# Performance work log

Measured on AMD Instinct MI355X. Metric: run time of the kernel, lower is better.

Reference implementation:

```python
import jax, jax.numpy as jnp
import numpy as np

B = 1024       # batch of triples
E = 50000      # num_entities
R = 500        # num_relations
D = 512        # dimension
P = 16         # parts
C = 8          # num_cores
ALPHA = 2.0    # -> q = alpha/2 = 1.0
Q = ALPHA / 2.0
DP = D // P    # 32


def setup_inputs() -> dict:
    key = jax.random.key(0)
    ks = jax.random.split(key, 10)
    xav_e = (2.0 / (E + D)) ** 0.5
    xav_r = (2.0 / (R + D)) ** 0.5
    return {
        "heads": jax.random.randint(ks[0], (B,), 0, E),
        "relations": jax.random.randint(ks[1], (B,), 0, R),
        "tails": jax.random.randint(ks[2], (B,), 0, E),
        "entity_w": jax.random.normal(ks[3], (E, D), dtype=jnp.float32) * xav_e,
        "relation_w": jax.random.normal(ks[4], (R, D), dtype=jnp.float32) * xav_r,
        "W_cores": jax.random.uniform(ks[5], (C, P, P, P), dtype=jnp.float32,
                                      minval=-0.01, maxval=0.01),
        "attn_w1": jax.random.normal(ks[6], (2 * D, D), dtype=jnp.float32) * (1.0 / (2 * D)) ** 0.5,
        "attn_b1": jnp.zeros((D,), dtype=jnp.float32),
        "attn_w2": jax.random.normal(ks[7], (D, C), dtype=jnp.float32) * (1.0 / D) ** 0.5,
        "attn_b2": jnp.zeros((C,), dtype=jnp.float32),
    }


def _pq_norm(x):
    # ((|x|^p).sum(2) ** q).sum(1), p=2
    return ((x * x).sum(2) ** Q).sum(1)


def _geometric_consistency(W_cores):
    # center of mass of |W| along each axis, per core; vectorized over cores
    coords = jnp.arange(P, dtype=jnp.float32)
    Wa = jnp.abs(W_cores)                      # [C,P,P,P]
    tot = Wa.sum(axis=(1, 2, 3))               # [C]
    cx = (Wa * coords[None, :, None, None]).sum(axis=(1, 2, 3)) / tot
    cy = (Wa * coords[None, None, :, None]).sum(axis=(1, 2, 3)) / tot
    cz = (Wa * coords[None, None, None, :]).sum(axis=(1, 2, 3)) / tot
    centers = jnp.stack([cx, cy, cz], axis=1)  # [C,3]
    d2 = ((centers[:, None, :] - centers[None, :, :]) ** 2).sum(-1)
    dist = jnp.sqrt(d2)
    masked = dist + jnp.eye(C, dtype=dist.dtype) * 1e6
    min_d = masked.min(axis=1)
    return -jnp.mean(jnp.log(min_d + 1e-6))


def reference(heads, relations, tails, entity_w, relation_w, W_cores,
              attn_w1, attn_b1, attn_w2, attn_b2):
    h = entity_w[heads]          # [B,D]
    r = relation_w[relations]    # [B,D]
    t = entity_w[tails]          # [B,D]

    hr = jnp.concatenate([h, r], axis=1)                       # [B,2D]
    hid = jax.nn.relu(hr @ attn_w1 + attn_b1)                  # [B,D]
    attn = jax.nn.softmax(hid @ attn_w2 + attn_b2, axis=1)     # [B,C]

    h3 = h.reshape(-1, DP, P)
    r3 = r.reshape(-1, DP, P)
    t3 = t.reshape(-1, DP, P)

    h_norm = _pq_norm(h3)
    r_norm = _pq_norm(r3)
    t_norm = _pq_norm(t3)

    # attention-weighted effective core per triple (sum over cores is linear,
    # so folding attn into W before the contraction is exactly the same math)
    Weff = jnp.einsum('bc,cpqs->bpqs', attn, W_cores)          # [B,P,P,P]

    # x1[b,i,s] = sum_{p,q} h[b,i,p] r[b,i,q] W[b,p,q,s]
    x1 = jnp.einsum('bip,biq,bpqs->bis', h3, r3, Weff)
    # x2[b,i,p] = sum_{q,s} r[b,i,q] t[b,i,s] W[b,p,q,s]
    x2 = jnp.einsum('biq,bis,bpqs->bip', r3, t3, Weff)
    # x3[b,i,q] = sum_{p,s} h[b,i,p] t[b,i,s] W[b,p,q,s]
    x3 = jnp.einsum('bip,bis,bpqs->biq', h3, t3, Weff)

    whr_norm = _pq_norm(x1)
    wrt_norm = _pq_norm(x2)
    wth_norm = _pq_norm(x3)

    scores = x1.reshape(-1, D) @ entity_w.T                    # [B,E]

    factor1 = jnp.mean(h_norm) + jnp.mean(r_norm) + jnp.mean(t_norm)
    factor2 = jnp.mean(whr_norm) + jnp.mean(wrt_norm) + jnp.mean(wth_norm)
    factor3 = _geometric_consistency(W_cores)
    return (scores, factor1, factor2, factor3, attn)
```

## Files before the change

kernel.cpp:

```cpp
#include <hip/hip_runtime.h>
#include <cstdint>
#include <cstddef>

#define NB 1024
#define NE 50000
#define NE_PAD 50048
#define DCOL 512
#define ATTN_C 8

static const size_t SCORES_OFF = (size_t)NB * NE;
static const size_t F1_OFF = SCORES_OFF + 0;
static const size_t F2_OFF = SCORES_OFF + 1;
static const size_t F3_OFF = SCORES_OFF + 2;
static const size_t ATTN_OFF = SCORES_OFF + 3;

typedef float f32x4 __attribute__((ext_vector_type(4)));
typedef short s16x8 __attribute__((ext_vector_type(8)));

__device__ __forceinline__ unsigned short f2bf(float f) {
  union { float f; uint32_t u; } x; x.f = f;
  uint32_t u = x.u;
  uint32_t r = (u + 0x7fffu + ((u >> 16) & 1u)) >> 16;
  return (unsigned short)r;
}

__device__ __forceinline__ void gload16(const void* g, void* l) {
  __builtin_amdgcn_global_load_lds(
      (const __attribute__((address_space(1))) uint32_t*)g,
      (__attribute__((address_space(3))) uint32_t*)l, 16, 0, 0);
}

template <int N>
__device__ __forceinline__ void waitcnt_vm() {
  static_assert(N == 0 || N == 4 || N == 8, "literal dispatch");
  if constexpr (N == 0) asm volatile("s_waitcnt vmcnt(0)" ::: "memory");
  else if constexpr (N == 4) asm volatile("s_waitcnt vmcnt(4)" ::: "memory");
  else if constexpr (N == 8) asm volatile("s_waitcnt vmcnt(8)" ::: "memory");
}

__global__ __launch_bounds__(256)
void prep(const int* __restrict__ heads, const int* __restrict__ rels,
          const int* __restrict__ tails, const float* __restrict__ ew,
          const float* __restrict__ rw, const float* __restrict__ w1,
          unsigned short* __restrict__ hrb, unsigned short* __restrict__ w1t,
          float* __restrict__ n1) {
  int tid = threadIdx.x;
  if (blockIdx.x < NB) {
    int b = blockIdx.x;
    const float* h = ew + (size_t)heads[b] * DCOL;
    const float* r = rw + (size_t)rels[b] * DCOL;
    const float* t = ew + (size_t)tails[b] * DCOL;
    float acc = 0.f;
    #pragma unroll
    for (int it = 0; it < 2; ++it) {
      int d = it * 256 + tid;
      float hv = h[d], rv = r[d], tv = t[d];
      hrb[(size_t)b * 1024 + d] = f2bf(hv);
      hrb[(size_t)b * 1024 + DCOL + d] = f2bf(rv);
      acc += hv * hv + rv * rv + tv * tv;
    }
    __shared__ float red[256];
    red[tid] = acc; __syncthreads();
    for (int s = 128; s > 0; s >>= 1) {
      if (tid < s) red[tid] += red[tid + s];
      __syncthreads();
    }
    if (tid == 0) n1[b] = red[0];
  } else {
    int tb = blockIdx.x - NB;
    int nb = (tb & 15) * 32, kb = (tb >> 4) * 32;
    __shared__ float tile[32][33];
    int tx = tid & 31, ty = tid >> 5;
    #pragma unroll
    for (int rr = 0; rr < 32; rr += 8)
      tile[ty + rr][tx] = w1[(size_t)(kb + ty + rr) * 512 + nb + tx];
    __syncthreads();
    #pragma unroll
    for (int rr = 0; rr < 32; rr += 8)
      w1t[(size_t)(nb + ty + rr) * 1024 + kb + tx] = f2bf(tile[tx][ty + rr]);
  }
}

template <int EPI, int WM, int WN, int FRm, int FRn, int SWZ, int MT, int CVT>
__global__ __launch_bounds__(WM * WN * 64, 2)
void gemm_nt(const unsigned short* __restrict__ A,
             const unsigned short* __restrict__ B,
             float* __restrict__ C, const float* __restrict__ bias,
             int K, int Nc, int NT,
             const float* __restrict__ cvt_src,
             unsigned short* __restrict__ cvt_dst, int ngemm) {
  constexpr int NW = WM * WN;
  constexpr int BM = WM * 16 * FRm;
  constexpr int BN = WN * 16 * FRn;
  constexpr int TILE_A = BM * 128;
  constexpr int TILE_B = BN * 128;
  constexpr int BUFSZ = TILE_A + TILE_B;
  constexpr int CPW_A = (BM / 8) / NW;
  constexpr int CPW_B = (BN / 8) / NW;
  constexpr int SOPS = CPW_A + CPW_B;
  static_assert((BM / 8) % NW == 0 && (BN / 8) % NW == 0, "chunk split");
  __shared__ __align__(16) uint8_t smem[2 * BUFSZ];
  const int tid = threadIdx.x;

  if (CVT && (int)blockIdx.x >= ngemm) {
    const int n4valid = NE * DCOL / 4;
    const int n4tot = NE_PAD * DCOL / 4;
    int i = ((int)blockIdx.x - ngemm) * (NW * 64) + tid;
    const int stride = ((int)gridDim.x - ngemm) * (NW * 64);
    for (; i < n4tot; i += stride) {
      float x = 0.f, y = 0.f, z = 0.f, w = 0.f;
      if (i < n4valid) {
        float4 v = ((const float4*)cvt_src)[i];
        x = v.x; y = v.y; z = v.z; w = v.w;
      }
      union { unsigned short u[4]; uint2 v2; } o;
      o.u[0] = f2bf(x); o.u[1] = f2bf(y); o.u[2] = f2bf(z); o.u[3] = f2bf(w);
      ((uint2*)cvt_dst)[i] = o.v2;
    }
    return;
  }

  const int lane = tid & 63;
  const int wv = tid >> 6;
  const int wm = wv / WN, wn = wv % WN;

  int m_t, n_t;
  if (SWZ) {
    int xcd = blockIdx.x & 7;
    int l = blockIdx.x >> 3;
    int w = xcd * ((MT * NT) >> 3) + l;
    n_t = w / MT; m_t = w % MT;
  } else {
    m_t = blockIdx.x % MT; n_t = blockIdx.x / MT;
  }
  const int m0 = m_t * BM;
  const int n0 = n_t * BN;
  const int rbytes = K * 2;

  f32x4 acc[FRm][FRn];
  #pragma unroll
  for (int i = 0; i < FRm; ++i)
    #pragma unroll
    for (int j = 0; j < FRn; ++j) acc[i][j] = (f32x4){0.f, 0.f, 0.f, 0.f};

  const int srow = lane >> 3;
  const int scol = lane & 7;
  const int nkt = K >> 6;

  auto stage = [&](int kt, int buf) {
    #pragma unroll
    for (int j = 0; j < CPW_A; ++j) {
      const int chunk = wv * CPW_A + j;
      const int r = chunk * 8 + srow;
      const int c = scol ^ (r & 7);
      gload16((const uint8_t*)A + (size_t)(m0 + r) * rbytes + kt * 128 + c * 16,
              &smem[buf * BUFSZ + chunk * 1024]);
    }
    #pragma unroll
    for (int j = 0; j < CPW_B; ++j) {
      const int chunk = wv * CPW_B + j;
      const int r = chunk * 8 + srow;
      const int c = scol ^ (r & 7);
      gload16((const uint8_t*)B + (size_t)(n0 + r) * rbytes + kt * 128 + c * 16,
              &smem[buf * BUFSZ + TILE_A + chunk * 1024]);
    }
  };
  auto compute = [&](int buf) {
    const uint8_t* sa = &smem[buf * BUFSZ];
    const uint8_t* sb = sa + TILE_A;
    #pragma unroll
    for (int kk = 0; kk < 2; ++kk) {
      s16x8 af[FRm], bfv[FRn];
      #pragma unroll
      for (int f = 0; f < FRm; ++f) {
        const int ra = (wm * FRm + f) * 16 + (lane & 15);
        const int ca = (kk * 4 + (lane >> 4)) ^ (ra & 7);
        af[f] = *(const s16x8*)&sa[ra * 128 + ca * 16];
      }
      #pragma unroll
      for (int f = 0; f < FRn; ++f) {
        const int rb = (wn * FRn + f) * 16 + (lane & 15);
        const int cb = (kk * 4 + (lane >> 4)) ^ (rb & 7);
        bfv[f] = *(const s16x8*)&sb[rb * 128 + cb * 16];
      }
      #pragma unroll
      for (int fm = 0; fm < FRm; ++fm)
        #pragma unroll
        for (int fn = 0; fn < FRn; ++fn)
          acc[fm][fn] = __builtin_amdgcn_mfma_f32_16x16x32_bf16(
              af[fm], bfv[fn], acc[fm][fn], 0, 0, 0);
    }
  };

  stage(0, 0);
  stage(1, 1);
  for (int kt = 0; kt < nkt - 1; ++kt) {
    const int cur = kt & 1;
    waitcnt_vm<SOPS>();
    __builtin_amdgcn_sched_barrier(0);
    __builtin_amdgcn_s_barrier();
    __builtin_amdgcn_sched_barrier(0);
    compute(cur);
    __builtin_amdgcn_sched_barrier(0);
    __builtin_amdgcn_s_barrier();
    __builtin_amdgcn_sched_barrier(0);
    if (kt + 2 < nkt) stage(kt + 2, cur);
  }
  waitcnt_vm<0>();
  __builtin_amdgcn_sched_barrier(0);
  __builtin_amdgcn_s_barrier();
  __builtin_amdgcn_sched_barrier(0);
  compute((nkt - 1) & 1);

  const int rl = lane >> 4, cl = lane & 15;
  #pragma unroll
  for (int fm = 0; fm < FRm; ++fm)
    #pragma unroll
    for (int fn = 0; fn < FRn; ++fn)
      #pragma unroll
      for (int j = 0; j < 4; ++j) {
        int gm = m0 + (wm * FRm + fm) * 16 + rl * 4 + j;
        int gn = n0 + (wn * FRn + fn) * 16 + cl;
        if (gn < Nc) {
          float v = acc[fm][fn][j];
          if (EPI) v = fmaxf(v + bias[gn], 0.f);
          C[(size_t)gm * Nc + gn] = v;
        }
      }
}

__global__ __launch_bounds__(256, 2)
void triple_core(const int* __restrict__ heads, const int* __restrict__ rels,
                 const int* __restrict__ tails, const float* __restrict__ ew,
                 const float* __restrict__ rw, const float* __restrict__ wc,
                 const float* __restrict__ hid, const float* __restrict__ w2,
                 const float* __restrict__ b2, float* __restrict__ attn_out,
                 unsigned short* __restrict__ x1b, float* __restrict__ n2) {
  __shared__ float hs[512], rs[512], ts[512];
  __shared__ __align__(16) float W123[4096][4];
  __shared__ float att[8];
  __shared__ float wred[4][8];
  __shared__ float red[256];
  int b = blockIdx.x, tid = threadIdx.x;
  int lane = tid & 63, wid = tid >> 6;
  const float* hp_ = ew + (size_t)heads[b] * DCOL;
  const float* rp_ = rw + (size_t)rels[b] * DCOL;
  const float* tp_ = ew + (size_t)tails[b] * DCOL;
  float la[8] = {0, 0, 0, 0, 0, 0, 0, 0};
  #pragma unroll
  for (int it = 0; it < 2; ++it) {
    int d = it * 256 + tid;
    hs[d] = hp_[d]; rs[d] = rp_[d]; ts[d] = tp_[d];
    float hv = hid[(size_t)b * DCOL + d];
    #pragma unroll
    for (int c = 0; c < 8; ++c) la[c] = fmaf(hv, w2[d * 8 + c], la[c]);
  }
  #pragma unroll
  for (int off = 32; off > 0; off >>= 1)
    #pragma unroll
    for (int c = 0; c < 8; ++c) la[c] += __shfl_down(la[c], off);
  if (lane == 0)
    #pragma unroll
    for (int c = 0; c < 8; ++c) wred[wid][c] = la[c];
  __syncthreads();
  if (tid == 0) {
    float lg[8];
    #pragma unroll
    for (int c = 0; c < 8; ++c)
      lg[c] = wred[0][c] + wred[1][c] + wred[2][c] + wred[3][c] + b2[c];
    float mx = lg[0];
    #pragma unroll
    for (int c = 1; c < 8; ++c) mx = fmaxf(mx, lg[c]);
    float e[8], s = 0.f;
    #pragma unroll
    for (int c = 0; c < 8; ++c) { e[c] = expf(lg[c] - mx); s += e[c]; }
    #pragma unroll
    for (int c = 0; c < 8; ++c) {
      float a = e[c] / s;
      att[c] = a;
      attn_out[(size_t)b * 8 + c] = a;
    }
  }
  __syncthreads();
  #pragma unroll
  for (int it = 0; it < 16; ++it) {
    int idx = it * 256 + tid;
    float w = 0.f;
    #pragma unroll
    for (int c = 0; c < 8; ++c) w = fmaf(att[c], wc[c * 4096 + idx], w);
    int s = idx & 15, q = (idx >> 4) & 15, p = idx >> 8;
    W123[idx][0] = w;
    W123[(q * 16 + s) * 16 + p][1] = w;
    W123[(p * 16 + s) * 16 + q][2] = w;
  }
  __syncthreads();

  const int so = tid & 15;
  const int i0 = tid >> 4, i1 = i0 + 16;
  float h0[16], r0[16], t0[16], h1[16], r1[16], t1[16];
  #pragma unroll
  for (int k = 0; k < 16; ++k) {
    h0[k] = hs[i0 * 16 + k]; r0[k] = rs[i0 * 16 + k]; t0[k] = ts[i0 * 16 + k];
    h1[k] = hs[i1 * 16 + k]; r1[k] = rs[i1 * 16 + k]; t1[k] = ts[i1 * 16 + k];
  }
  float a10 = 0.f, a20 = 0.f, a30 = 0.f, a11 = 0.f, a21 = 0.f, a31 = 0.f;
  const float4* wp = (const float4*)&W123[so][0];
  #pragma unroll
  for (int u = 0; u < 16; ++u) {
    #pragma unroll
    for (int v = 0; v < 16; ++v) {
      float4 w = wp[u * 256 + v * 16];
      a10 = fmaf(h0[u] * r0[v], w.x, a10);
      a20 = fmaf(r0[u] * t0[v], w.y, a20);
      a30 = fmaf(h0[u] * t0[v], w.z, a30);
      a11 = fmaf(h1[u] * r1[v], w.x, a11);
      a21 = fmaf(r1[u] * t1[v], w.y, a21);
      a31 = fmaf(h1[u] * t1[v], w.z, a31);
    }
  }
  x1b[(size_t)b * 512 + i0 * 16 + so] = f2bf(a10);
  x1b[(size_t)b * 512 + i1 * 16 + so] = f2bf(a11);
  red[tid] = a10 * a10 + a20 * a20 + a30 * a30
           + a11 * a11 + a21 * a21 + a31 * a31;
  __syncthreads();
  for (int s = 128; s > 0; s >>= 1) {
    if (tid < s) red[tid] += red[tid + s];
    __syncthreads();
  }
  if (tid == 0) n2[b] = red[0];
}

__global__ __launch_bounds__(256)
void finalize(const float* __restrict__ n1, const float* __restrict__ n2,
              const float* __restrict__ wc, float* __restrict__ out) {
  int tid = threadIdx.x;
  __shared__ float red[256];
  float a = 0.f;
  for (int i = tid; i < NB; i += 256) a += n1[i];
  red[tid] = a; __syncthreads();
  for (int s = 128; s > 0; s >>= 1) { if (tid < s) red[tid] += red[tid + s]; __syncthreads(); }
  if (tid == 0) out[F1_OFF] = red[0] / (float)NB;
  __syncthreads();
  a = 0.f;
  for (int i = tid; i < NB; i += 256) a += n2[i];
  red[tid] = a; __syncthreads();
  for (int s = 128; s > 0; s >>= 1) { if (tid < s) red[tid] += red[tid + s]; __syncthreads(); }
  if (tid == 0) out[F2_OFF] = red[0] / (float)NB;
  __syncthreads();

  int c = tid >> 5, l = tid & 31;
  float tot = 0.f, cx = 0.f, cy = 0.f, cz = 0.f;
  for (int e = l; e < 4096; e += 32) {
    float w = fabsf(wc[c * 4096 + e]);
    int z = e & 15, y = (e >> 4) & 15, x = e >> 8;
    tot += w; cx += w * x; cy += w * y; cz += w * z;
  }
  #pragma unroll
  for (int off = 16; off > 0; off >>= 1) {
    tot += __shfl_down(tot, off);
    cx += __shfl_down(cx, off);
    cy += __shfl_down(cy, off);
    cz += __shfl_down(cz, off);
  }
  __shared__ float cent[8][3];
  if (l == 0) { cent[c][0] = cx / tot; cent[c][1] = cy / tot; cent[c][2] = cz / tot; }
  __syncthreads();
  if (tid == 0) {
    float f3 = 0.f;
    for (int i = 0; i < 8; ++i) {
      float mn = 1e30f;
      for (int j = 0; j < 8; ++j) {
        if (j == i) continue;
        float dx = cent[i][0] - cent[j][0];
        float dy = cent[i][1] - cent[j][1];
        float dz = cent[i][2] - cent[j][2];
        float d = sqrtf(dx * dx + dy * dy + dz * dz);
        mn = fminf(mn, d);
      }
      f3 += logf(mn + 1e-6f);
    }
    out[F3_OFF] = -f3 / 8.f;
  }
}

extern "C" void kernel_launch(void* const* d_in, const int* in_sizes, int n_in,
                              void* d_out, int out_size, void* d_ws, size_t ws_size,
                              hipStream_t stream) {
  const int* heads = (const int*)d_in[0];
  const int* rels = (const int*)d_in[1];
  const int* tails = (const int*)d_in[2];
  const float* ew = (const float*)d_in[3];
  const float* rw = (const float*)d_in[4];
  const float* wc = (const float*)d_in[5];
  const float* w1 = (const float*)d_in[6];
  const float* b1 = (const float*)d_in[7];
  const float* w2 = (const float*)d_in[8];
  const float* b2 = (const float*)d_in[9];
  float* out = (float*)d_out;

  uint8_t* ws = (uint8_t*)d_ws;
  const size_t EWB_SZ = (size_t)NE_PAD * DCOL * 2;
  unsigned short* ewb = (unsigned short*)ws;
  unsigned short* hrb = (unsigned short*)(ws + EWB_SZ);
  unsigned short* w1t = (unsigned short*)(ws + EWB_SZ + 2097152);
  float* hid = (float*)(ws + EWB_SZ + 2097152 + 1048576);
  unsigned short* x1b = (unsigned short*)(ws + EWB_SZ + 2097152 + 1048576 + 2097152);
  float* n1 = (float*)(ws + EWB_SZ + 2097152 + 1048576 + 2097152 + 1048576);
  float* n2 = n1 + NB;

  prep<<<NB + 512, 256, 0, stream>>>(heads, rels, tails, ew, rw, w1,
                                     hrb, w1t, n1);
  gemm_nt<1, 2, 2, 2, 2, 0, 16, 1><<<128 + 2048, 256, 0, stream>>>(
      hrb, w1t, hid, b1, 1024, 512, 8, ew, ewb, 128);
  triple_core<<<NB, 256, 0, stream>>>(heads, rels, tails, ew, rw, wc,
                                      hid, w2, b2, out + ATTN_OFF, x1b, n2);
  gemm_nt<0, 2, 2, 4, 4, 1, 8, 0><<<3128, 256, 0, stream>>>(
      x1b, ewb, out, nullptr, 512, NE, 391, nullptr, nullptr, 0);
  finalize<<<1, 256, 0, stream>>>(n1, n2, wc, out);
}
```

Before: 214.8 us.

## Generalize GEMM pipeline depth, make K compile-time, narrow score-GEMM tile

The GEMM kernel gains template parameters for pipeline depth and total K, so the K loop fully unrolls and wait counts are compile-time constants. The scores GEMM moves to a 3-stage LDS pipeline with the N tile halved (FRn 4→2), which doubles the grid to 6256 blocks. The aim is to hide more global-load latency and improve load balance and occupancy on the large output GEMM. In exchange it uses more LDS per block and reuses each A tile less per block.

```diff
diff --git a/kernel.cpp b/kernel.cpp
--- a/kernel.cpp
+++ b/kernel.cpp
@@ -32,10 +32,12 @@
 
 template <int N>
 __device__ __forceinline__ void waitcnt_vm() {
-  static_assert(N == 0 || N == 4 || N == 8, "literal dispatch");
+  static_assert(N == 0 || N == 4 || N == 6 || N == 8 || N == 12, "literal");
   if constexpr (N == 0) asm volatile("s_waitcnt vmcnt(0)" ::: "memory");
   else if constexpr (N == 4) asm volatile("s_waitcnt vmcnt(4)" ::: "memory");
+  else if constexpr (N == 6) asm volatile("s_waitcnt vmcnt(6)" ::: "memory");
   else if constexpr (N == 8) asm volatile("s_waitcnt vmcnt(8)" ::: "memory");
+  else if constexpr (N == 12) asm volatile("s_waitcnt vmcnt(12)" ::: "memory");
 }
 
 __global__ __launch_bounds__(256)
@@ -81,12 +83,13 @@
   }
 }
 
-template <int EPI, int WM, int WN, int FRm, int FRn, int SWZ, int MT, int CVT>
+template <int EPI, int WM, int WN, int FRm, int FRn, int SWZ, int MT, int CVT,
+          int DEPTH, int KTOT>
 __global__ __launch_bounds__(WM * WN * 64, 2)
 void gemm_nt(const unsigned short* __restrict__ A,
              const unsigned short* __restrict__ B,
              float* __restrict__ C, const float* __restrict__ bias,
-             int K, int Nc, int NT,
+             int Nc, int NT,
              const float* __restrict__ cvt_src,
              unsigned short* __restrict__ cvt_dst, int ngemm) {
   constexpr int NW = WM * WN;
@@ -98,8 +101,11 @@
   constexpr int CPW_A = (BM / 8) / NW;
   constexpr int CPW_B = (BN / 8) / NW;
   constexpr int SOPS = CPW_A + CPW_B;
+  constexpr int NKT = KTOT / 64;
+  constexpr int RBY = KTOT * 2;
   static_assert((BM / 8) % NW == 0 && (BN / 8) % NW == 0, "chunk split");
-  __shared__ __align__(16) uint8_t smem[2 * BUFSZ];
+  static_assert(NKT >= DEPTH, "pipeline deeper than K");
+  __shared__ __align__(16) uint8_t smem[DEPTH * BUFSZ];
   const int tid = threadIdx.x;
 
   if (CVT && (int)blockIdx.x >= ngemm) {
@@ -135,7 +141,6 @@
   }
   const int m0 = m_t * BM;
   const int n0 = n_t * BN;
-  const int rbytes = K * 2;
 
   f32x4 acc[FRm][FRn];
   #pragma unroll
@@ -145,7 +150,6 @@
 
   const int srow = lane >> 3;
   const int scol = lane & 7;
-  const int nkt = K >> 6;
 
   auto stage = [&](int kt, int buf) {
     #pragma unroll
@@ -153,7 +157,7 @@
       const int chunk = wv * CPW_A + j;
       const int r = chunk * 8 + srow;
       const int c = scol ^ (r & 7);
-      gload16((const uint8_t*)A + (size_t)(m0 + r) * rbytes + kt * 128 + c * 16,
+      gload16((const uint8_t*)A + (size_t)(m0 + r) * RBY + kt * 128 + c * 16,
               &smem[buf * BUFSZ + chunk * 1024]);
     }
     #pragma unroll
@@ -161,7 +165,7 @@
       const int chunk = wv * CPW_B + j;
       const int r = chunk * 8 + srow;
       const int c = scol ^ (r & 7);
-      gload16((const uint8_t*)B + (size_t)(n0 + r) * rbytes + kt * 128 + c * 16,
+      gload16((const uint8_t*)B + (size_t)(n0 + r) * RBY + kt * 128 + c * 16,
               &smem[buf * BUFSZ + TILE_A + chunk * 1024]);
     }
   };
@@ -192,25 +196,27 @@
     }
   };
 
-  stage(0, 0);
-  stage(1, 1);
-  for (int kt = 0; kt < nkt - 1; ++kt) {
-    const int cur = kt & 1;
-    waitcnt_vm<SOPS>();
+  #pragma unroll
+  for (int d = 0; d < DEPTH; ++d) stage(d, d);
+
+  #pragma unroll
+  for (int kt = 0; kt < NKT; ++kt) {
+    const int rem = NKT - 1 - kt;
+    const int w = (rem < DEPTH - 1 ? rem : DEPTH - 1) * SOPS;
+    if (w == 12) waitcnt_vm<12>();
+    else if (w == 8) waitcnt_vm<8>();
+    else if (w == 6) waitcnt_vm<6>();
+    else if (w == 4) waitcnt_vm<4>();
+    else waitcnt_vm<0>();
     __builtin_amdgcn_sched_barrier(0);
     __builtin_amdgcn_s_barrier();
     __builtin_amdgcn_sched_barrier(0);
-    compute(cur);
+    compute(kt % DEPTH);
     __builtin_amdgcn_sched_barrier(0);
     __builtin_amdgcn_s_barrier();
     __builtin_amdgcn_sched_barrier(0);
-    if (kt + 2 < nkt) stage(kt + 2, cur);
-  }
-  waitcnt_vm<0>();
-  __builtin_amdgcn_sched_barrier(0);
-  __builtin_amdgcn_s_barrier();
-  __builtin_amdgcn_sched_barrier(0);
-  compute((nkt - 1) & 1);
+    if (kt + DEPTH < NKT) stage(kt + DEPTH, kt % DEPTH);
+  }
 
   const int rl = lane >> 4, cl = lane & 15;
   #pragma unroll
@@ -410,11 +416,11 @@
 
   prep<<<NB + 512, 256, 0, stream>>>(heads, rels, tails, ew, rw, w1,
                                      hrb, w1t, n1);
-  gemm_nt<1, 2, 2, 2, 2, 0, 16, 1><<<128 + 2048, 256, 0, stream>>>(
-      hrb, w1t, hid, b1, 1024, 512, 8, ew, ewb, 128);
+  gemm_nt<1, 2, 2, 2, 2, 0, 16, 1, 2, 1024><<<128 + 2048, 256, 0, stream>>>(
+      hrb, w1t, hid, b1, 512, 8, ew, ewb, 128);
   triple_core<<<NB, 256, 0, stream>>>(heads, rels, tails, ew, rw, wc,
                                       hid, w2, b2, out + ATTN_OFF, x1b, n2);
-  gemm_nt<0, 2, 2, 4, 4, 1, 8, 0><<<3128, 256, 0, stream>>>(
-      x1b, ewb, out, nullptr, 512, NE, 391, nullptr, nullptr, 0);
+  gemm_nt<0, 2, 2, 4, 2, 1, 8, 0, 3, 512><<<6256, 256, 0, stream>>>(
+      x1b, ewb, out, nullptr, NE, 782, nullptr, nullptr, 0);
   finalize<<<1, 256, 0, stream>>>(n1, n2, wc, out);
 }
```

New measurement: 218.6 us. Within noise of the previous version (+1.8%).

## Add dedicated triple-buffered 128x256 scores GEMM with 8 waves and setprio

Applied to the files above, without the earlier changes.

Replaces the generic scores GEMM with a specialized kernel that uses 512 threads, 128x256 tiles, and a three-stage LDS ring. The next stage is issued before computing the current one, and s_setprio is raised around the MFMA section. K is made a compile-time constant so the loops fully unroll, and the entity padding grows to a multiple of 256. The aim is more data reuse per tile and better overlap of global loads with MFMA work, at the cost of heavy LDS use (144 KB) that allows only one block per CU.

```diff
diff --git a/kernel.cpp b/kernel.cpp
--- a/kernel.cpp
+++ b/kernel.cpp
@@ -4,7 +4,7 @@
 
 #define NB 1024
 #define NE 50000
-#define NE_PAD 50048
+#define NE_PAD 50176
 #define DCOL 512
 #define ATTN_C 8
 
@@ -32,9 +32,10 @@
 
 template <int N>
 __device__ __forceinline__ void waitcnt_vm() {
-  static_assert(N == 0 || N == 4 || N == 8, "literal dispatch");
+  static_assert(N == 0 || N == 4 || N == 6 || N == 8, "literal");
   if constexpr (N == 0) asm volatile("s_waitcnt vmcnt(0)" ::: "memory");
   else if constexpr (N == 4) asm volatile("s_waitcnt vmcnt(4)" ::: "memory");
+  else if constexpr (N == 6) asm volatile("s_waitcnt vmcnt(6)" ::: "memory");
   else if constexpr (N == 8) asm volatile("s_waitcnt vmcnt(8)" ::: "memory");
 }
 
@@ -81,12 +82,13 @@
   }
 }
 
-template <int EPI, int WM, int WN, int FRm, int FRn, int SWZ, int MT, int CVT>
+template <int EPI, int WM, int WN, int FRm, int FRn, int SWZ, int MT, int CVT,
+          int KTOT>
 __global__ __launch_bounds__(WM * WN * 64, 2)
 void gemm_nt(const unsigned short* __restrict__ A,
              const unsigned short* __restrict__ B,
              float* __restrict__ C, const float* __restrict__ bias,
-             int K, int Nc, int NT,
+             int Nc, int NT,
              const float* __restrict__ cvt_src,
              unsigned short* __restrict__ cvt_dst, int ngemm) {
   constexpr int NW = WM * WN;
@@ -98,6 +100,8 @@
   constexpr int CPW_A = (BM / 8) / NW;
   constexpr int CPW_B = (BN / 8) / NW;
   constexpr int SOPS = CPW_A + CPW_B;
+  constexpr int NKT = KTOT / 64;
+  constexpr int RBY = KTOT * 2;
   static_assert((BM / 8) % NW == 0 && (BN / 8) % NW == 0, "chunk split");
   __shared__ __align__(16) uint8_t smem[2 * BUFSZ];
   const int tid = threadIdx.x;
@@ -135,7 +139,6 @@
   }
   const int m0 = m_t * BM;
   const int n0 = n_t * BN;
-  const int rbytes = K * 2;
 
   f32x4 acc[FRm][FRn];
   #pragma unroll
@@ -145,7 +148,6 @@
 
   const int srow = lane >> 3;
   const int scol = lane & 7;
-  const int nkt = K >> 6;
 
   auto stage = [&](int kt, int buf) {
     #pragma unroll
@@ -153,7 +155,7 @@
       const int chunk = wv * CPW_A + j;
       const int r = chunk * 8 + srow;
       const int c = scol ^ (r & 7);
-      gload16((const uint8_t*)A + (size_t)(m0 + r) * rbytes + kt * 128 + c * 16,
+      gload16((const uint8_t*)A + (size_t)(m0 + r) * RBY + kt * 128 + c * 16,
               &smem[buf * BUFSZ + chunk * 1024]);
     }
     #pragma unroll
@@ -161,7 +163,7 @@
       const int chunk = wv * CPW_B + j;
       const int r = chunk * 8 + srow;
       const int c = scol ^ (r & 7);
-      gload16((const uint8_t*)B + (size_t)(n0 + r) * rbytes + kt * 128 + c * 16,
+      gload16((const uint8_t*)B + (size_t)(n0 + r) * RBY + kt * 128 + c * 16,
               &smem[buf * BUFSZ + TILE_A + chunk * 1024]);
     }
   };
@@ -194,7 +196,7 @@
 
   stage(0, 0);
   stage(1, 1);
-  for (int kt = 0; kt < nkt - 1; ++kt) {
+  for (int kt = 0; kt < NKT - 1; ++kt) {
     const int cur = kt & 1;
     waitcnt_vm<SOPS>();
     __builtin_amdgcn_sched_barrier(0);
@@ -204,13 +206,13 @@
     __builtin_amdgcn_sched_barrier(0);
     __builtin_amdgcn_s_barrier();
     __builtin_amdgcn_sched_barrier(0);
-    if (kt + 2 < nkt) stage(kt + 2, cur);
+    if (kt + 2 < NKT) stage(kt + 2, cur);
   }
   waitcnt_vm<0>();
   __builtin_amdgcn_sched_barrier(0);
   __builtin_amdgcn_s_barrier();
   __builtin_amdgcn_sched_barrier(0);
-  compute((nkt - 1) & 1);
+  compute((NKT - 1) & 1);
 
   const int rl = lane >> 4, cl = lane & 15;
   #pragma unroll
@@ -226,6 +228,108 @@
           if (EPI) v = fmaxf(v + bias[gn], 0.f);
           C[(size_t)gm * Nc + gn] = v;
         }
+      }
+}
+
+__global__ __launch_bounds__(512, 1)
+void gemm_scores(const unsigned short* __restrict__ A,
+                 const unsigned short* __restrict__ B,
+                 float* __restrict__ C, int Nc, int NT) {
+  constexpr int TILE_A = 128 * 128;
+  constexpr int TILE_B = 256 * 128;
+  constexpr int BUFSZ = TILE_A + TILE_B;
+  constexpr int NKT = 8;
+  constexpr int RBY = 1024;
+  __shared__ __align__(16) uint8_t smem[3 * BUFSZ];
+  const int tid = threadIdx.x;
+  const int lane = tid & 63;
+  const int wv = tid >> 6;
+  const int wm = wv >> 2, wn = wv & 3;
+
+  const int xcd = blockIdx.x & 7;
+  const int l = blockIdx.x >> 3;
+  const int w = xcd * NT + l;
+  const int n_t = w >> 3, m_t = w & 7;
+  const int m0 = m_t * 128;
+  const int n0 = n_t * 256;
+
+  f32x4 acc[4][4];
+  #pragma unroll
+  for (int i = 0; i < 4; ++i)
+    #pragma unroll
+    for (int j = 0; j < 4; ++j) acc[i][j] = (f32x4){0.f, 0.f, 0.f, 0.f};
+
+  const int srow = lane >> 3;
+  const int scol = lane & 7;
+
+  auto stage = [&](int kt, int buf) {
+    #pragma unroll
+    for (int j = 0; j < 2; ++j) {
+      const int chunk = wv * 2 + j;
+      const int r = chunk * 8 + srow;
+      const int c = scol ^ (r & 7);
+      gload16((const uint8_t*)A + (size_t)(m0 + r) * RBY + kt * 128 + c * 16,
+              &smem[buf * BUFSZ + chunk * 1024]);
+    }
+    #pragma unroll
+    for (int j = 0; j < 4; ++j) {
+      const int chunk = wv * 4 + j;
+      const int r = chunk * 8 + srow;
+      const int c = scol ^ (r & 7);
+      gload16((const uint8_t*)B + (size_t)(n0 + r) * RBY + kt * 128 + c * 16,
+              &smem[buf * BUFSZ + TILE_A + chunk * 1024]);
+    }
+  };
+  auto compute = [&](int buf) {
+    const uint8_t* sa = &smem[buf * BUFSZ];
+    const uint8_t* sb = sa + TILE_A;
+    __builtin_amdgcn_s_setprio(1);
+    #pragma unroll
+    for (int kk = 0; kk < 2; ++kk) {
+      s16x8 af[4], bfv[4];
+      #pragma unroll
+      for (int f = 0; f < 4; ++f) {
+        const int ra = wm * 64 + f * 16 + (lane & 15);
+        const int ca = (kk * 4 + (lane >> 4)) ^ (ra & 7);
+        af[f] = *(const s16x8*)&sa[ra * 128 + ca * 16];
+        const int rb = wn * 64 + f * 16 + (lane & 15);
+        const int cb = (kk * 4 + (lane >> 4)) ^ (rb & 7);
+        bfv[f] = *(const s16x8*)&sb[rb * 128 + cb * 16];
+      }
+      #pragma unroll
+      for (int fm = 0; fm < 4; ++fm)
+        #pragma unroll
+        for (int fn = 0; fn < 4; ++fn)
+          acc[fm][fn] = __builtin_amdgcn_mfma_f32_16x16x32_bf16(
+              af[fm], bfv[fn], acc[fm][fn], 0, 0, 0);
+    }
+    __builtin_amdgcn_s_setprio(0);
+  };
+
+  stage(0, 0);
+  stage(1, 1);
+  #pragma unroll
+  for (int kt = 0; kt < NKT; ++kt) {
+    if (kt < NKT - 1) waitcnt_vm<6>();
+    else waitcnt_vm<0>();
+    __builtin_amdgcn_sched_barrier(0);
+    __builtin_amdgcn_s_barrier();
+    __builtin_amdgcn_sched_barrier(0);
+    if (kt + 2 < NKT) stage(kt + 2, (kt + 2) % 3);
+    __builtin_amdgcn_sched_barrier(0);
+    compute(kt % 3);
+  }
+
+  const int rl = lane >> 4, cl = lane & 15;
+  #pragma unroll
+  for (int fm = 0; fm < 4; ++fm)
+    #pragma unroll
+    for (int fn = 0; fn < 4; ++fn)
+      #pragma unroll
+      for (int j = 0; j < 4; ++j) {
+        int gm = m0 + wm * 64 + fm * 16 + rl * 4 + j;
+        int gn = n0 + wn * 64 + fn * 16 + cl;
+        if (gn < Nc) C[(size_t)gm * Nc + gn] = acc[fm][fn][j];
       }
 }
 
@@ -410,11 +514,10 @@
 
   prep<<<NB + 512, 256, 0, stream>>>(heads, rels, tails, ew, rw, w1,
                                      hrb, w1t, n1);
-  gemm_nt<1, 2, 2, 2, 2, 0, 16, 1><<<128 + 2048, 256, 0, stream>>>(
-      hrb, w1t, hid, b1, 1024, 512, 8, ew, ewb, 128);
+  gemm_nt<1, 2, 2, 2, 2, 0, 16, 1, 1024><<<128 + 2048, 256, 0, stream>>>(
+      hrb, w1t, hid, b1, 512, 8, ew, ewb, 128);
   triple_core<<<NB, 256, 0, stream>>>(heads, rels, tails, ew, rw, wc,
                                       hid, w2, b2, out + ATTN_OFF, x1b, n2);
-  gemm_nt<0, 2, 2, 4, 4, 1, 8, 0><<<3128, 256, 0, stream>>>(
-      x1b, ewb, out, nullptr, 512, NE, 391, nullptr, nullptr, 0);
+  gemm_scores<<<1568, 512, 0, stream>>>(x1b, ewb, out, NE, 196);
   finalize<<<1, 256, 0, stream>>>(n1, n2, wc, out);
 }
```

Result: no change. 216.2 us (+0.7%).
